# Optimization experiments

Measured on AMD Instinct MI355X. Metric: run time of the kernel, lower is better.

## Reference

```python
import jax, jax.numpy as jnp
import numpy as np

VOCAB = 50257
H = 512  # output_size == embed dim == lstm hidden
N = 65536  # number of tokens


def setup_inputs() -> dict:
    key = jax.random.key(0)
    ks = jax.random.split(key, 12)
    s = 1.0 / np.sqrt(H)  # torch LSTM/Linear init scale
    inp = {
        "ids": jax.random.randint(ks[0], (N,), 0, VOCAB, dtype=jnp.int64)
        if jax.config.jax_enable_x64 else jax.random.randint(ks[0], (N,), 0, VOCAB, dtype=jnp.int32),
        "emb": jax.random.normal(ks[1], (VOCAB, H), dtype=jnp.float32),
        # LSTM layer 0 (gate order: i, f, g, o)
        "W_ih0": jax.random.uniform(ks[2], (4 * H, H), jnp.float32, -s, s),
        "W_hh0": jax.random.uniform(ks[3], (4 * H, H), jnp.float32, -s, s),
        "b_ih0": jax.random.uniform(ks[4], (4 * H,), jnp.float32, -s, s),
        "b_hh0": jax.random.uniform(ks[5], (4 * H,), jnp.float32, -s, s),
        # LSTM layer 1
        "W_ih1": jax.random.uniform(ks[6], (4 * H, H), jnp.float32, -s, s),
        "W_hh1": jax.random.uniform(ks[7], (4 * H, H), jnp.float32, -s, s),
        "b_ih1": jax.random.uniform(ks[8], (4 * H,), jnp.float32, -s, s),
        "b_hh1": jax.random.uniform(ks[9], (4 * H,), jnp.float32, -s, s),
        # final Linear
        "W_lin": jax.random.uniform(ks[10], (H, H), jnp.float32, -s, s),
        "b_lin": jax.random.uniform(ks[11], (H,), jnp.float32, -s, s),
    }
    return inp


def _lstm_cell_zero_state(x, W_ih, b_ih, b_hh):
    # Single LSTM step with h_prev = c_prev = 0, so W_hh @ h_prev == 0.
    # gates: [N, 4H] in torch order i, f, g, o
    gates = x @ W_ih.T + (b_ih + b_hh)
    i, f, g, o = jnp.split(gates, 4, axis=-1)
    c = jax.nn.sigmoid(i) * jnp.tanh(g)  # f * c_prev == 0
    h = jax.nn.sigmoid(o) * jnp.tanh(c)
    return h


def reference(ids, emb, W_ih0, W_hh0, b_ih0, b_hh0, W_ih1, W_hh1, b_ih1, b_hh1, W_lin, b_lin):
    # Each token is processed with a fresh zero LSTM state, so the python
    # loop in the original vectorizes exactly over the token dim.
    x = emb[ids]                                   # [N, H]
    h0 = _lstm_cell_zero_state(x, W_ih0, b_ih0, b_hh0)   # layer 1 hidden
    h1 = _lstm_cell_zero_state(h0, W_ih1, b_ih1, b_hh1)  # layer 2 hidden (hidden[-1])
    out = jax.nn.relu(h1 @ W_lin.T + b_lin)        # [N, H]
    return out[:, None, :]                         # stacked [N, 1, H] like torch.stack of [1,H]
```

## Files before the change

kernel.cpp:

```cpp
#include <hip/hip_runtime.h>
#include <stdint.h>


typedef _Float16 half8 __attribute__((ext_vector_type(8)));
typedef __attribute__((ext_vector_type(4))) float float4v;
typedef __attribute__((ext_vector_type(4))) unsigned int uint4v;

__device__ __forceinline__ float sigmoidf_(float x) { return 1.0f / (1.0f + __expf(-x)); }
__device__ __forceinline__ float tanhf_(float x) { return 1.0f - 2.0f / (__expf(2.0f * x) + 1.0f); }

__device__ __forceinline__ void gl2lds16(const void* g, void* l) {
  __builtin_amdgcn_global_load_lds(
      (const __attribute__((address_space(1))) void*)g,
      (__attribute__((address_space(3))) void*)l, 16, 0, 0);
}

__global__ __launch_bounds__(256) void prep_kernel(
    const float* __restrict__ emb,
    const float* __restrict__ W0, const float* __restrict__ bi0, const float* __restrict__ bh0,
    const float* __restrict__ W1, const float* __restrict__ bi1, const float* __restrict__ bh1,
    const float* __restrict__ WL,
    _Float16* __restrict__ Ef,
    _Float16* __restrict__ W0f, _Float16* __restrict__ W1f, _Float16* __restrict__ WLf,
    float* __restrict__ b0p, float* __restrict__ b1p)
{
  int id = blockIdx.x * 256 + threadIdx.x;
  if (id < 3216448) {
    const float* s = emb + (size_t)id * 8;
    float4v v0 = *(const float4v*)s;
    float4v v1 = *(const float4v*)(s + 4);
    union { _Float16 h[8]; uint4v u; } P;
#pragma unroll
    for (int e = 0; e < 4; ++e) { P.h[e] = (_Float16)v0[e]; P.h[4 + e] = (_Float16)v1[e]; }
    *(uint4v*)(Ef + (size_t)id * 8) = P.u;
  } else if (id < 3347520) {
    int u = id - 3216448;
    int np = u >> 6, k0 = (u & 63) << 3;
    int n = ((np & 3) << 9) | (np >> 2);
    const float* s = W0 + n * 512 + k0;
    float4v v0 = *(const float4v*)s;
    float4v v1 = *(const float4v*)(s + 4);
    union { _Float16 h[8]; uint4v u; } P;
#pragma unroll
    for (int e = 0; e < 4; ++e) { P.h[e] = (_Float16)v0[e]; P.h[4 + e] = (_Float16)v1[e]; }
    *(uint4v*)(W0f + np * 512 + k0) = P.u;
  } else if (id < 3478592) {
    int u = id - 3347520;
    int np = u >> 6, k0 = (u & 63) << 3;
    int n = ((np & 3) << 9) | (np >> 2);
    const float* s = W1 + n * 512 + k0;
    float4v v0 = *(const float4v*)s;
    float4v v1 = *(const float4v*)(s + 4);
    union { _Float16 h[8]; uint4v u; } P;
#pragma unroll
    for (int e = 0; e < 4; ++e) { P.h[e] = (_Float16)v0[e]; P.h[4 + e] = (_Float16)v1[e]; }
    *(uint4v*)(W1f + np * 512 + k0) = P.u;
  } else if (id < 3511360) {
    int u = id - 3478592;
    const float* s = WL + (size_t)u * 8;
    float4v v0 = *(const float4v*)s;
    float4v v1 = *(const float4v*)(s + 4);
    union { _Float16 h[8]; uint4v u8; } P;
#pragma unroll
    for (int e = 0; e < 4; ++e) { P.h[e] = (_Float16)v0[e]; P.h[4 + e] = (_Float16)v1[e]; }
    *(uint4v*)(WLf + (size_t)u * 8) = P.u8;
  } else if (id < 3513408) {
    int np = id - 3511360;
    int n = ((np & 3) << 9) | (np >> 2);
    b0p[np] = bi0[n] + bh0[n];
  } else if (id < 3515456) {
    int np = id - 3513408;
    int n = ((np & 3) << 9) | (np >> 2);
    b1p[np] = bi1[n] + bh1[n];
  } else if (id < 3526656) {
    int u = id - 3515456;
    *(uint4v*)(Ef + 25731584 + (size_t)u * 8) = (uint4v){0u, 0u, 0u, 0u};
  }
}

template <int MODE>
__global__ __launch_bounds__(512, 4) void gemm_kernel(
    const _Float16* __restrict__ A, const int* __restrict__ ids,
    const _Float16* __restrict__ B, const float* __restrict__ bias,
    _Float16* __restrict__ Of, float* __restrict__ Out,
    int nbShift, int nbMask)
{
  __shared__ __align__(16) char smem[65536];
  const int T = threadIdx.x;
  const int lane = T & 63;
  const int wv = T >> 6;
  const int wrow = wv >> 1, wcol = wv & 1;
  const int nwg = (int)gridDim.x;
  const int bid = (int)blockIdx.x;
  const int swz = (bid & 7) * (nwg >> 3) + (bid >> 3);
  const int mb = swz >> nbShift;
  const int nb = swz & nbMask;
  const size_t t0 = (size_t)mb * 256;
  const int n0 = nb * 128;

  const int r0 = T >> 2;
  const int qg = (T & 3) ^ ((r0 >> 1) & 3);
  size_t sr0 = t0 + r0, sr1 = t0 + 128 + r0;
  if (ids) { sr0 = (size_t)(unsigned)ids[sr0]; sr1 = (size_t)(unsigned)ids[sr1]; }
  const _Float16* gA0 = A + sr0 * 512 + qg * 8;
  const _Float16* gA1 = A + sr1 * 512 + qg * 8;
  const _Float16* gB  = B + (size_t)(n0 + r0) * 512 + qg * 8;

  const int d0 = T * 16;
#define STAGE(dst) do { \
    gl2lds16(gA0, (dst) + d0); \
    gl2lds16(gA1, (dst) + 8192 + d0); \
    gl2lds16(gB,  (dst) + 16384 + d0); \
    gA0 += 32; gA1 += 32; gB += 32; } while (0)

  const int m_ = lane & 15, qf = lane >> 4;
  const int qs = qf ^ ((m_ >> 1) & 3);
  const int offA = wrow * 2048 + m_ * 32 + qs * 8;
  const int offB = 8192 + wcol * 2048 + m_ * 32 + qs * 8;

  float4v acc[4][4];
#pragma unroll
  for (int i = 0; i < 4; ++i)
#pragma unroll
    for (int j = 0; j < 4; ++j)
      acc[i][j] = (float4v){0.f, 0.f, 0.f, 0.f};

  char* bufc = smem;
  char* bufn = smem + 32768;
  STAGE(bufc);

  for (int it = 0; it < 16; ++it) {
    if (it < 15) {
      STAGE(bufn);
      asm volatile("s_waitcnt vmcnt(3)" ::: "memory");
    } else {
      asm volatile("s_waitcnt vmcnt(0)" ::: "memory");
    }
    __builtin_amdgcn_sched_barrier(0);
    __builtin_amdgcn_s_barrier();

    const _Float16* cur = (const _Float16*)bufc;
    half8 a[4], b[4];
#pragma unroll
    for (int i = 0; i < 4; ++i) {
      a[i] = *(const half8*)(cur + offA + i * 512);
      b[i] = *(const half8*)(cur + offB + i * 512);
    }
#pragma unroll
    for (int i = 0; i < 4; ++i)
#pragma unroll
      for (int j = 0; j < 4; ++j)
        acc[i][j] = __builtin_amdgcn_mfma_f32_16x16x32_f16(b[j], a[i], acc[i][j], 0, 0, 0);
    __builtin_amdgcn_sched_barrier(0);
    __builtin_amdgcn_s_barrier();
    __builtin_amdgcn_sched_barrier(0);
    char* tc = bufc; bufc = bufn; bufn = tc;
  }
#undef STAGE

  float4v bq[4];
#pragma unroll
  for (int j = 0; j < 4; ++j)
    bq[j] = *(const float4v*)(bias + n0 + wcol * 64 + j * 16 + qf * 4);

  if (MODE == 0) {
    _Float16* hT = (_Float16*)smem;
    const int ub = wcol * 16 + qf;
#pragma unroll
    for (int i = 0; i < 4; ++i) {
      const int trow = wrow * 64 + i * 16 + m_;
#pragma unroll
      for (int j = 0; j < 4; ++j) {
        float yi = acc[i][j][0] + bq[j][0];
        float yg = acc[i][j][2] + bq[j][2];
        float yo = acc[i][j][3] + bq[j][3];
        float cc = sigmoidf_(yi) * tanhf_(yg);
        float hh = sigmoidf_(yo) * tanhf_(cc);
        hT[trow * 40 + ub + j * 4] = (_Float16)hh;
      }
    }
    __syncthreads();
    const int tl = T >> 1, hf = T & 1;
    const _Float16* src = hT + tl * 40 + hf * 16;
    uint4v v0 = *(const uint4v*)(src);
    uint4v v1 = *(const uint4v*)(src + 8);
    _Float16* dst = Of + (t0 + tl) * 512 + (size_t)(nb * 32) + hf * 16;
    *(uint4v*)dst = v0;
    *(uint4v*)(dst + 8) = v1;
  } else {
#pragma unroll
    for (int i = 0; i < 4; ++i) {
      const size_t row = t0 + wrow * 64 + i * 16 + m_;
#pragma unroll
      for (int j = 0; j < 4; ++j) {
        float4v v;
#pragma unroll
        for (int r2 = 0; r2 < 4; ++r2)
          v[r2] = fmaxf(acc[i][j][r2] + bq[j][r2], 0.0f);
        *(float4v*)(Out + row * 512 + (size_t)(n0 + wcol * 64 + j * 16 + qf * 4)) = v;
      }
    }
  }
}

extern "C" void kernel_launch(void* const* d_in, const int* in_sizes, int n_in,
                              void* d_out, int out_size, void* d_ws, size_t ws_size,
                              hipStream_t stream) {
  (void)in_sizes; (void)n_in; (void)out_size; (void)ws_size;
  const int*   ids   = (const int*)d_in[0];
  const float* emb   = (const float*)d_in[1];
  const float* W0    = (const float*)d_in[2];
  const float* bi0   = (const float*)d_in[4];
  const float* bh0   = (const float*)d_in[5];
  const float* W1    = (const float*)d_in[6];
  const float* bi1   = (const float*)d_in[8];
  const float* bh1   = (const float*)d_in[9];
  const float* WL    = (const float*)d_in[10];
  const float* blin  = (const float*)d_in[11];
  float* out = (float*)d_out;

  char* ws = (char*)d_ws;
  const size_t MB = 1024 * 1024;
  _Float16* W0f = (_Float16*)(ws);
  _Float16* W1f = (_Float16*)(ws + 2 * MB);
  _Float16* WLf = (_Float16*)(ws + 4 * MB);
  float*    b0p = (float*)(ws + 4 * MB + 512 * 1024);
  float*    b1p = (float*)(ws + 4 * MB + 512 * 1024 + 8192);
  _Float16* Ef  = (_Float16*)(ws + 8 * MB);
  _Float16* H1f = Ef;
  _Float16* H0f = (_Float16*)(ws + 72 * MB);

  prep_kernel<<<13776, 256, 0, stream>>>(emb, W0, bi0, bh0, W1, bi1, bh1, WL,
                                         Ef, W0f, W1f, WLf, b0p, b1p);
  gemm_kernel<0><<<3152, 512, 0, stream>>>(Ef, nullptr, W0f, b0p, H0f, nullptr, 4, 15);
  gemm_kernel<0><<<3152, 512, 0, stream>>>(H0f, nullptr, W1f, b1p, H1f, nullptr, 4, 15);
  gemm_kernel<1><<<1024, 512, 0, stream>>>(H1f, ids, WLf, blin, nullptr, out, 2, 3);
}
```

Measured before the change: 541.1 us.

## Replace final linear GEMM with full-width 128-row tile kernel

Swaps the final Linear+ReLU launch for a dedicated kernel in which each block computes 128 rows across all 512 output columns. Each gathered activation row is then loaded once rather than once per column tile. The new kernel drops double buffering, uses a single LDS buffer with two syncthreads per k-step, and holds 32 accumulators per thread at one block per CU. It launches 512 blocks, so occupancy is lower and load latency is more exposed.

New measurement: 569.9 us. 1.05x slower.

```diff
diff --git a/kernel.cpp b/kernel.cpp
--- a/kernel.cpp
+++ b/kernel.cpp
@@ -203,6 +203,81 @@
   }
 }
 
+__global__ __launch_bounds__(512, 1) void gemm1_kernel(
+    const _Float16* __restrict__ A, const int* __restrict__ ids,
+    const _Float16* __restrict__ B, const float* __restrict__ bias,
+    float* __restrict__ Out)
+{
+  __shared__ __align__(16) char smem[40960];
+  _Float16* sA = (_Float16*)smem;
+
+  const int T = threadIdx.x;
+  const int lane = T & 63;
+  const int wcol = T >> 6;
+  const size_t t0 = (size_t)blockIdx.x * 128;
+
+  const int r0 = T >> 2;
+  const int qg = (T & 3) ^ ((r0 >> 1) & 3);
+  const size_t sr = (size_t)(unsigned)ids[t0 + r0];
+  const _Float16* gA  = A + sr * 512 + qg * 8;
+  const _Float16* gB0 = B + (size_t)(r0)       * 512 + qg * 8;
+  const _Float16* gB1 = B + (size_t)(128 + r0) * 512 + qg * 8;
+  const _Float16* gB2 = B + (size_t)(256 + r0) * 512 + qg * 8;
+  const _Float16* gB3 = B + (size_t)(384 + r0) * 512 + qg * 8;
+
+  const int m_ = lane & 15, qf = lane >> 4;
+  const int qs = qf ^ ((m_ >> 1) & 3);
+  const int offA = m_ * 32 + qs * 8;
+  const int offB = 4096 + (wcol * 64 + m_) * 32 + qs * 8;
+
+  float4v acc[8][4];
+#pragma unroll
+  for (int i = 0; i < 8; ++i)
+#pragma unroll
+    for (int j = 0; j < 4; ++j)
+      acc[i][j] = (float4v){0.f, 0.f, 0.f, 0.f};
+
+  for (int it = 0; it < 16; ++it) {
+    gl2lds16(gA,  smem + T * 16);
+    gl2lds16(gB0, smem + 8192  + T * 16);
+    gl2lds16(gB1, smem + 16384 + T * 16);
+    gl2lds16(gB2, smem + 24576 + T * 16);
+    gl2lds16(gB3, smem + 32768 + T * 16);
+    gA += 32; gB0 += 32; gB1 += 32; gB2 += 32; gB3 += 32;
+    __syncthreads();
+
+    half8 a[8], b[4];
+#pragma unroll
+    for (int i = 0; i < 8; ++i) a[i] = *(const half8*)(sA + offA + i * 512);
+#pragma unroll
+    for (int j = 0; j < 4; ++j) b[j] = *(const half8*)(sA + offB + j * 512);
+#pragma unroll
+    for (int i = 0; i < 8; ++i)
+#pragma unroll
+      for (int j = 0; j < 4; ++j)
+        acc[i][j] = __builtin_amdgcn_mfma_f32_16x16x32_f16(b[j], a[i], acc[i][j], 0, 0, 0);
+    __syncthreads();
+  }
+
+  float4v bq[4];
+#pragma unroll
+  for (int j = 0; j < 4; ++j)
+    bq[j] = *(const float4v*)(bias + wcol * 64 + j * 16 + qf * 4);
+
+#pragma unroll
+  for (int i = 0; i < 8; ++i) {
+    const size_t row = t0 + i * 16 + m_;
+#pragma unroll
+    for (int j = 0; j < 4; ++j) {
+      float4v v;
+#pragma unroll
+      for (int r2 = 0; r2 < 4; ++r2)
+        v[r2] = fmaxf(acc[i][j][r2] + bq[j][r2], 0.0f);
+      *(float4v*)(Out + row * 512 + (size_t)(wcol * 64 + j * 16 + qf * 4)) = v;
+    }
+  }
+}
+
 extern "C" void kernel_launch(void* const* d_in, const int* in_sizes, int n_in,
                               void* d_out, int out_size, void* d_ws, size_t ws_size,
                               hipStream_t stream) {
@@ -234,5 +309,5 @@
                                          Ef, W0f, W1f, WLf, b0p, b1p);
   gemm_kernel<0><<<3152, 512, 0, stream>>>(Ef, nullptr, W0f, b0p, H0f, nullptr, 4, 15);
   gemm_kernel<0><<<3152, 512, 0, stream>>>(H0f, nullptr, W1f, b1p, H1f, nullptr, 4, 15);
-  gemm_kernel<1><<<1024, 512, 0, stream>>>(H1f, ids, WLf, blin, nullptr, out, 2, 3);
-}
+  gemm1_kernel<<<512, 512, 0, stream>>>(H1f, ids, WLf, blin, out);
+}
```
